# Optimization experiments

Hardware: AMD Instinct MI355X
Metric: run time of the kernel (lower is better)

The kernel has to match this reference:

```python
import jax, jax.numpy as jnp
import numpy as np

K = 3          # kernel size
PAD = 1        # padding


def _conv2d(x, w, b):
    # plain 3x3 conv, stride 1, pad 1, NCHW / OIHW
    out = jax.lax.conv_general_dilated(
        x, w, window_strides=(1, 1), padding=((PAD, PAD), (PAD, PAD)),
        dimension_numbers=('NCHW', 'OIHW', 'NCHW'))
    return out + b[None, :, None, None]


def _deform_conv2d(x, offsets, w, b):
    # torchvision deform_conv2d semantics (stride=1, dilation=1, no mask)
    B, C, H, W = x.shape
    K2 = K * K
    off = offsets.reshape(B, K2, 2, H, W)
    dy, dx = off[:, :, 0], off[:, :, 1]              # [B,K2,H,W], (y,x) order
    ki, kj = jnp.meshgrid(jnp.arange(K), jnp.arange(K), indexing='ij')
    ki = ki.reshape(K2).astype(x.dtype)
    kj = kj.reshape(K2).astype(x.dtype)
    base_y = (jnp.arange(H, dtype=x.dtype)[None, :, None] - PAD + ki[:, None, None])  # [K2,H,1]
    base_x = (jnp.arange(W, dtype=x.dtype)[None, None, :] - PAD + kj[:, None, None])  # [K2,1,W]
    py = base_y[None] + dy                            # [B,K2,H,W] sampling rows
    px = base_x[None] + dx                            # [B,K2,H,W] sampling cols

    y0 = jnp.floor(py); x0 = jnp.floor(px)
    y1 = y0 + 1.0;      x1 = x0 + 1.0
    wy1 = py - y0; wy0 = 1.0 - wy1
    wx1 = px - x0; wx0 = 1.0 - wx1

    def corner(yc, xc, wgt):
        valid = ((yc >= 0) & (yc <= H - 1) & (xc >= 0) & (xc <= W - 1))
        iy = jnp.clip(yc, 0, H - 1).astype(jnp.int32)
        ix = jnp.clip(xc, 0, W - 1).astype(jnp.int32)
        # per-batch gather: x[b][:, iy[b], ix[b]] -> [C,K2,H,W]
        vals = jax.vmap(lambda xb, iyb, ixb: xb[:, iyb, ixb])(x, iy, ix)
        return vals * (wgt * valid.astype(x.dtype))[:, None]  # [B,C,K2,H,W]

    sampled = (corner(y0, x0, wy0 * wx0) + corner(y0, x1, wy0 * wx1)
               + corner(y1, x0, wy1 * wx0) + corner(y1, x1, wy1 * wx1))
    out = jnp.einsum('bckhw,ock->bohw', sampled, w.reshape(w.shape[0], C, K2))
    return out + b[None, :, None, None]


def setup_inputs() -> dict:
    key = jax.random.key(0)
    ks = jax.random.split(key, 6)
    B, C, O, H, W = 4, 256, 256, 64, 64
    x = jax.random.normal(ks[0], (B, C, H, W), dtype=jnp.float32)
    y = jax.random.normal(ks[1], (B, C, H, W), dtype=jnp.float32)
    # offset conv predicts 2*K*K offset channels; small init keeps offsets a few px
    offset_w = jax.random.normal(ks[2], (2 * K * K, C, K, K), dtype=jnp.float32) * 0.01
    offset_b = jax.random.normal(ks[3], (2 * K * K,), dtype=jnp.float32) * 0.01
    deform_w = jax.random.normal(ks[4], (O, C, K, K), dtype=jnp.float32) * (1.0 / np.sqrt(C * K * K))
    deform_b = jax.random.normal(ks[5], (O,), dtype=jnp.float32) * 0.01
    return {"x": x, "y": y, "offset_w": offset_w, "offset_b": offset_b,
            "deform_w": deform_w, "deform_b": deform_b}


def reference(x, y, offset_w, offset_b, deform_w, deform_b):
    offsets = _conv2d(y, offset_w, offset_b)          # [B, 2*K*K, H, W]
    return _deform_conv2d(x, offsets, deform_w, deform_b)
```

## Files before the change

### kernel.cpp

```cpp
#include <hip/hip_runtime.h>
#include <hip/hip_bf16.h>
#include <stdint.h>


typedef __bf16 bf16x8 __attribute__((ext_vector_type(8)));
typedef float  f32x4  __attribute__((ext_vector_type(4)));

__device__ __forceinline__ unsigned short f2bfu(float f) {
    union { float f; unsigned u; } v; v.f = f;
    return (unsigned short)((v.u + 0x8000u) >> 16);
}
__device__ __forceinline__ float lo16(unsigned u) {
    union { unsigned u; float f; } v; v.u = u << 16; return v.f;
}
__device__ __forceinline__ float hi16(unsigned u) {
    union { unsigned u; float f; } v; v.u = u & 0xFFFF0000u; return v.f;
}
__device__ __forceinline__ unsigned fbits(float f) {
    union { float f; unsigned u; } v; v.f = f; return v.u;
}
__device__ __forceinline__ unsigned blend2(unsigned u0, unsigned u1, unsigned u2, unsigned u3,
                                           float4 w) {
    float lo = w.x * lo16(u0) + w.y * lo16(u1) + w.z * lo16(u2) + w.w * lo16(u3);
    float hi = w.x * hi16(u0) + w.y * hi16(u1) + w.z * hi16(u2) + w.w * hi16(u3);
    unsigned rl = fbits(lo) + 0x8000u;
    unsigned rh = fbits(hi) + 0x8000u;
    return __builtin_amdgcn_perm(rh, rl, 0x07060302);
}

__global__ __launch_bounds__(256) void xpose2_kernel(const float* __restrict__ x,
                                                     const float* __restrict__ y,
                                                     unsigned short* __restrict__ xT,
                                                     unsigned short* __restrict__ yT) {
    __shared__ float tile[64 * 69];
    int blk = blockIdx.x;
    const float* src = x; unsigned short* dst = xT;
    if (blk >= 1024) { src = y; dst = yT; blk -= 1024; }
    int cq = blk & 3;
    int bh = blk >> 2;
    int t = threadIdx.x;
    int w4 = t & 15, cl0 = t >> 4;
    const float* s = src + ((size_t)(bh >> 6) * 256 + cq * 64) * 4096 + (size_t)(bh & 63) * 64;
#pragma unroll
    for (int p = 0; p < 4; ++p) {
        int cl = p * 16 + cl0;
        float4 v = *(const float4*)&s[(size_t)cl * 4096 + w4 * 4];
        tile[(w4 * 4 + 0) * 69 + cl] = v.x;
        tile[(w4 * 4 + 1) * 69 + cl] = v.y;
        tile[(w4 * 4 + 2) * 69 + cl] = v.z;
        tile[(w4 * 4 + 3) * 69 + cl] = v.w;
    }
    __syncthreads();
    unsigned short* d = dst + (size_t)bh * 16384 + cq * 64;
#pragma unroll
    for (int p = 0; p < 4; ++p) {
        int w = p * 16 + cl0;
        float4 v = *(const float4*)&tile[w * 69 + w4 * 4];
        ushort4 r = make_ushort4(f2bfu(v.x), f2bfu(v.y), f2bfu(v.z), f2bfu(v.w));
        *(ushort4*)&d[w * 256 + w4 * 4] = r;
    }
}

__global__ __launch_bounds__(256) void packw_kernel(const float* __restrict__ dw,
                                                    unsigned short* __restrict__ Wp2) {
    int tid = blockIdx.x * 256 + threadIdx.x;
    int q8 = tid >> 8;
    int o  = tid & 255;
    int k0 = q8 * 8;
    int tap = k0 >> 8, c0 = k0 & 255;
    const float* s = dw + o * 2304 + c0 * 9 + tap;
    ushort4 r0 = make_ushort4(f2bfu(s[0]), f2bfu(s[9]), f2bfu(s[18]), f2bfu(s[27]));
    ushort4 r1 = make_ushort4(f2bfu(s[36]), f2bfu(s[45]), f2bfu(s[54]), f2bfu(s[63]));
    *(ushort4*)&Wp2[tid * 8 + 0] = r0;
    *(ushort4*)&Wp2[tid * 8 + 4] = r1;
}

__global__ __launch_bounds__(256) void packow_kernel(const float* __restrict__ ow,
                                                     unsigned short* __restrict__ Bo) {
    int idx = blockIdx.x * 256 + threadIdx.x;
    int j = idx & 7;
    int n = (idx >> 3) & 31;
    int lq = (idx >> 8) & 3;
    int kg = idx >> 10;
    int k = kg * 32 + lq * 8 + j;
    int tap = k >> 8, c = k & 255;
    float v = (n < 18) ? ow[n * 2304 + c * 9 + tap] : 0.f;
    Bo[idx] = f2bfu(v);
}

__global__ __launch_bounds__(512) void offs_mfma_kernel(
    const unsigned short* __restrict__ yT,
    const unsigned short* __restrict__ Bo,
    const float* __restrict__ ob,
    float* __restrict__ offs)
{
    __shared__ unsigned short yr[3 * 66 * 256];
    float* red = (float*)yr;

    int blk = blockIdx.x;
    int b = blk >> 6, h = blk & 63;
    int t = threadIdx.x;

#pragma unroll
    for (int r = 0; r < 3; ++r) {
        int hr = h + r - 1;
        bool rowok = (hr >= 0) && (hr < 64);
        const unsigned short* src = yT + (size_t)(b * 64 + (hr & 63)) * 64 * 256;
        for (int g = t; g < 2112; g += 512) {
            int wp = g >> 5, gi = g & 31;
            uint4 v = make_uint4(0, 0, 0, 0);
            if (rowok && wp >= 1 && wp <= 64)
                v = *(const uint4*)&src[(wp - 1) * 256 + gi * 8];
            *(uint4*)&yr[(r * 66 + wp) * 256 + (gi ^ (wp & 7)) * 8] = v;
        }
    }
    __syncthreads();

    int wv = t >> 6, lane = t & 63;
    int mh = wv & 1, kq = wv >> 1;
    int ln = lane & 15, lq = lane >> 4;

    f32x4 acc[2][2];
#pragma unroll
    for (int ms = 0; ms < 2; ++ms)
#pragma unroll
        for (int nt = 0; nt < 2; ++nt)
            acc[ms][nt] = (f32x4){0.f, 0.f, 0.f, 0.f};

    for (int u = kq; u < 72; u += 4) {
        int tap = u >> 3, kc = u & 7;
        int ki = tap / 3, kj = tap - ki * 3;
        int gb = kc * 4 + lq;
        bf16x8 af[2];
#pragma unroll
        for (int ms = 0; ms < 2; ++ms) {
            int wp = mh * 32 + ms * 16 + ln + kj;
            af[ms] = *(const bf16x8*)&yr[(ki * 66 + wp) * 256 + (gb ^ (wp & 7)) * 8];
        }
        bf16x8 bfr[2];
#pragma unroll
        for (int nt = 0; nt < 2; ++nt)
            bfr[nt] = *(const bf16x8*)&Bo[(tap * 8 + kc) * 1024 + lq * 256 + (nt * 16 + ln) * 8];
#pragma unroll
        for (int ms = 0; ms < 2; ++ms)
#pragma unroll
            for (int nt = 0; nt < 2; ++nt)
                acc[ms][nt] = __builtin_amdgcn_mfma_f32_16x16x32_bf16(af[ms], bfr[nt], acc[ms][nt], 0, 0, 0);
    }

    __syncthreads();
    if (kq > 0) {
        float* rg = red + (size_t)((mh * 3 + (kq - 1)) * 4) * 256;
#pragma unroll
        for (int ms = 0; ms < 2; ++ms)
#pragma unroll
            for (int nt = 0; nt < 2; ++nt)
#pragma unroll
                for (int r = 0; r < 4; ++r)
                    rg[(ms * 2 + nt) * 256 + (lq * 4 + r) * 16 + ln] = acc[ms][nt][r];
    }
    __syncthreads();
    if (kq == 0) {
#pragma unroll
        for (int ms = 0; ms < 2; ++ms)
#pragma unroll
            for (int nt = 0; nt < 2; ++nt) {
                int o = nt * 16 + ln;
                f32x4 s = acc[ms][nt];
#pragma unroll
                for (int kk = 0; kk < 3; ++kk) {
                    const float* rg = red + (size_t)((mh * 3 + kk) * 4 + ms * 2 + nt) * 256;
#pragma unroll
                    for (int r = 0; r < 4; ++r)
                        s[r] += rg[(lq * 4 + r) * 16 + ln];
                }
                if (o < 18) {
                    float bias = ob[o];
                    float* dst = offs + ((size_t)b * 18 + o) * 4096 + h * 64 + mh * 32 + ms * 16 + lq * 4;
                    float4 st = make_float4(s[0] + bias, s[1] + bias, s[2] + bias, s[3] + bias);
                    *(float4*)dst = st;
                }
            }
    }
}

__device__ __forceinline__ void gather_tap(const unsigned short* __restrict__ xtb,
                                           unsigned short* __restrict__ buf,
                                           const float4* __restrict__ pw_lds,
                                           const int4* __restrict__ pi_lds,
                                           int tap, int wv, int lane) {
    int p2 = lane >> 5, cl = lane & 31;
    int c0 = cl * 8;
    int base = tap * 64 + wv * 2 + p2;
    float4 w = pw_lds[base];
    int4  pi = pi_lds[base];
    uint4 a00 = *(const uint4*)&xtb[pi.x + c0];
    uint4 a01 = *(const uint4*)&xtb[pi.y + c0];
    uint4 a10 = *(const uint4*)&xtb[pi.z + c0];
    uint4 a11 = *(const uint4*)&xtb[pi.w + c0];
#pragma unroll
    for (int i = 0; i < 4; ++i) {
        uint4 b00, b01, b10, b11; float4 wn; int4 pin;
        if (i < 3) {
            wn  = pw_lds[base + (i + 1) * 16];
            pin = pi_lds[base + (i + 1) * 16];
            b00 = *(const uint4*)&xtb[pin.x + c0];
            b01 = *(const uint4*)&xtb[pin.y + c0];
            b10 = *(const uint4*)&xtb[pin.z + c0];
            b11 = *(const uint4*)&xtb[pin.w + c0];
        }
        int pos = i * 16 + wv * 2 + p2;
        uint4 res;
        res.x = blend2(a00.x, a01.x, a10.x, a11.x, w);
        res.y = blend2(a00.y, a01.y, a10.y, a11.y, w);
        res.z = blend2(a00.z, a01.z, a10.z, a11.z, w);
        res.w = blend2(a00.w, a01.w, a10.w, a11.w, w);
        *(uint4*)&buf[pos * 256 + (cl ^ (pos & 7)) * 8] = res;
        if (i < 3) { a00 = b00; a01 = b01; a10 = b10; a11 = b11; w = wn; pi = pin; }
    }
}

__global__ __launch_bounds__(512, 2) void deform_kernel(
    const unsigned short* __restrict__ xT,
    const unsigned short* __restrict__ Wp2,
    const float* __restrict__ offs,
    const float* __restrict__ db,
    float* __restrict__ out)
{
    __shared__ unsigned char smem[86016];
    unsigned short* Abuf0 = (unsigned short*)smem;
    unsigned short* Abuf1 = (unsigned short*)(smem + 32768);
    float* epi = (float*)smem;
    float4* pw_lds = (float4*)(smem + 67584);
    int4*   pi_lds = (int4*)(smem + 67584 + 9216);

    int blk = blockIdx.x;
    int b = blk >> 6, h = blk & 63;
    int t = threadIdx.x;
    int wv = t >> 6, lane = t & 63;
    int ln = lane & 15, lq = lane >> 4;
    int ns = wv & 3, kh = wv >> 2;

    const unsigned short* xtb = xT + (size_t)b * (64 * 64 * 256);
    const float* offb = offs + (size_t)b * 18 * 4096 + h * 64;

    for (int job = t; job < 576; job += 512) {
        int tap = job >> 6, pos = job & 63;
        int ki = tap / 3, kj = tap - ki * 3;
        float dy = offb[(tap * 2 + 0) * 4096 + pos];
        float dx = offb[(tap * 2 + 1) * 4096 + pos];
        float py = (float)(h - 1 + ki) + dy;
        float px = (float)(pos - 1 + kj) + dx;
        float y0 = floorf(py), x0 = floorf(px);
        float wy1 = py - y0, wx1 = px - x0;
        float wy0 = 1.f - wy1, wx0 = 1.f - wx1;
        float y1 = y0 + 1.f, x1 = x0 + 1.f;
        float vy0 = (y0 >= 0.f && y0 <= 63.f) ? 1.f : 0.f;
        float vy1 = (y1 >= 0.f && y1 <= 63.f) ? 1.f : 0.f;
        float vx0 = (x0 >= 0.f && x0 <= 63.f) ? 1.f : 0.f;
        float vx1 = (x1 >= 0.f && x1 <= 63.f) ? 1.f : 0.f;
        int iy0 = (int)fminf(fmaxf(y0, 0.f), 63.f);
        int iy1 = (int)fminf(fmaxf(y1, 0.f), 63.f);
        int ix0 = (int)fminf(fmaxf(x0, 0.f), 63.f);
        int ix1 = (int)fminf(fmaxf(x1, 0.f), 63.f);
        pw_lds[job] = make_float4(wy0 * wx0 * vy0 * vx0, wy0 * wx1 * vy0 * vx1,
                                  wy1 * wx0 * vy1 * vx0, wy1 * wx1 * vy1 * vx1);
        pi_lds[job] = make_int4((iy0 * 64 + ix0) * 256, (iy0 * 64 + ix1) * 256,
                                (iy1 * 64 + ix0) * 256, (iy1 * 64 + ix1) * 256);
    }
    __syncthreads();

    f32x4 acc[4][4];
#pragma unroll
    for (int ms = 0; ms < 4; ++ms)
#pragma unroll
        for (int nt = 0; nt < 4; ++nt)
            acc[ms][nt] = (f32x4){0.f, 0.f, 0.f, 0.f};

    gather_tap(xtb, Abuf0, pw_lds, pi_lds, 0, wv, lane);
    __syncthreads();

    for (int tap = 0; tap < 9; ++tap) {
        if (tap < 8)
            gather_tap(xtb, ((tap + 1) & 1) ? Abuf1 : Abuf0, pw_lds, pi_lds, tap + 1, wv, lane);
        const unsigned short* Ab = (tap & 1) ? Abuf1 : Abuf0;
#pragma unroll
        for (int kc = 0; kc < 4; ++kc) {
            int gbase = kh * 16 + kc * 4 + lq;
            bf16x8 af[4];
#pragma unroll
            for (int ms = 0; ms < 4; ++ms) {
                int row = ms * 16 + ln;
                af[ms] = *(const bf16x8*)&Ab[row * 256 + (gbase ^ (row & 7)) * 8];
            }
            int kg = tap * 8 + kh * 4 + kc;
            bf16x8 bfr[4];
#pragma unroll
            for (int nt = 0; nt < 4; ++nt)
                bfr[nt] = *(const bf16x8*)&Wp2[((kg * 4 + lq) * 256 + ns * 64 + nt * 16 + ln) * 8];
#pragma unroll
            for (int ms = 0; ms < 4; ++ms)
#pragma unroll
                for (int nt = 0; nt < 4; ++nt)
                    acc[ms][nt] = __builtin_amdgcn_mfma_f32_16x16x32_bf16(af[ms], bfr[nt], acc[ms][nt], 0, 0, 0);
        }
        __syncthreads();
    }

    if (kh == 1) {
        float* e = epi + (size_t)ns * 4224;
#pragma unroll
        for (int ms = 0; ms < 4; ++ms)
#pragma unroll
            for (int nt = 0; nt < 4; ++nt) {
                int o_l = nt * 16 + ln;
                int wb = ms * 16 + lq * 4;
                f32x4 a = acc[ms][nt];
                float4 st = make_float4(a[0], a[1], a[2], a[3]);
                *(float4*)&e[o_l * 66 + wb] = st;
            }
    }
    __syncthreads();
    if (kh == 0) {
        const float* e = epi + (size_t)ns * 4224;
#pragma unroll
        for (int ms = 0; ms < 4; ++ms)
#pragma unroll
            for (int nt = 0; nt < 4; ++nt) {
                int o_l = nt * 16 + ln;
                int o = ns * 64 + o_l;
                int wb = ms * 16 + lq * 4;
                float bias = db[o];
                float4 p = *(const float4*)&e[o_l * 66 + wb];
                f32x4 a = acc[ms][nt];
                float4 st = make_float4(a[0] + p.x + bias, a[1] + p.y + bias,
                                        a[2] + p.z + bias, a[3] + p.w + bias);
                *(float4*)&out[((size_t)(b * 256 + o)) * 4096 + h * 64 + wb] = st;
            }
    }
}

extern "C" void kernel_launch(void* const* d_in, const int* in_sizes, int n_in,
                              void* d_out, int out_size, void* d_ws, size_t ws_size,
                              hipStream_t stream) {
    const float* x  = (const float*)d_in[0];
    const float* y  = (const float*)d_in[1];
    const float* ow = (const float*)d_in[2];
    const float* ob = (const float*)d_in[3];
    const float* dw = (const float*)d_in[4];
    const float* db = (const float*)d_in[5];
    float* out = (float*)d_out;

    char* ws = (char*)d_ws;
    unsigned short* xT  = (unsigned short*)(ws);
    unsigned short* yT  = (unsigned short*)(ws + 8388608);
    unsigned short* Wp2 = (unsigned short*)(ws + 16777216);
    unsigned short* Bo  = (unsigned short*)(ws + 16777216 + 1179648);
    float*          offs = (float*)(ws + 16777216 + 1179648 + 147456);

    hipLaunchKernelGGL(xpose2_kernel, dim3(2048), dim3(256), 0, stream, x, y, xT, yT);
    hipLaunchKernelGGL(packw_kernel, dim3(288), dim3(256), 0, stream, dw, Wp2);
    hipLaunchKernelGGL(packow_kernel, dim3(288), dim3(256), 0, stream, ow, Bo);
    hipLaunchKernelGGL(offs_mfma_kernel, dim3(256), dim3(512), 0, stream, yT, Bo, ob, offs);
    hipLaunchKernelGGL(deform_kernel, dim3(256), dim3(512), 0, stream, xT, Wp2, offs, db, out);
}
```

Baseline: 144.3 us.

## Split rows into half-row blocks, merge prep kernels, restructure gather pipelining

Merges the transpose and weight-packing kernels into one prep launch. Both the offset conv and the deform conv now work on half-row tiles (32 positions), doubling the grid to 512 blocks with a swizzled block order, raising launch bounds to 4 blocks per CU and shrinking LDS use. The deform gather is split into an issue phase (global loads into registers before the MFMA loop) and a commit phase (blend and LDS write after it), so gather latency overlaps with compute. The epilogue uses an XOR-swizzled LDS layout. The trade-off is more tap-halo reloads per block and higher register pressure from holding the gathered values across the MFMA loop.

```diff
diff --git a/kernel.cpp b/kernel.cpp
--- a/kernel.cpp
+++ b/kernel.cpp
@@ -28,214 +28,190 @@
     return __builtin_amdgcn_perm(rh, rl, 0x07060302);
 }
 
-__global__ __launch_bounds__(256) void xpose2_kernel(const float* __restrict__ x,
-                                                     const float* __restrict__ y,
-                                                     unsigned short* __restrict__ xT,
-                                                     unsigned short* __restrict__ yT) {
+__global__ __launch_bounds__(256) void prep_kernel(
+    const float* __restrict__ x, const float* __restrict__ y,
+    const float* __restrict__ ow, const float* __restrict__ dw,
+    unsigned short* __restrict__ xT, unsigned short* __restrict__ yT,
+    unsigned short* __restrict__ Wp2, unsigned short* __restrict__ Bo)
+{
     __shared__ float tile[64 * 69];
     int blk = blockIdx.x;
-    const float* src = x; unsigned short* dst = xT;
-    if (blk >= 1024) { src = y; dst = yT; blk -= 1024; }
-    int cq = blk & 3;
-    int bh = blk >> 2;
     int t = threadIdx.x;
-    int w4 = t & 15, cl0 = t >> 4;
-    const float* s = src + ((size_t)(bh >> 6) * 256 + cq * 64) * 4096 + (size_t)(bh & 63) * 64;
-#pragma unroll
-    for (int p = 0; p < 4; ++p) {
-        int cl = p * 16 + cl0;
-        float4 v = *(const float4*)&s[(size_t)cl * 4096 + w4 * 4];
-        tile[(w4 * 4 + 0) * 69 + cl] = v.x;
-        tile[(w4 * 4 + 1) * 69 + cl] = v.y;
-        tile[(w4 * 4 + 2) * 69 + cl] = v.z;
-        tile[(w4 * 4 + 3) * 69 + cl] = v.w;
-    }
-    __syncthreads();
-    unsigned short* d = dst + (size_t)bh * 16384 + cq * 64;
-#pragma unroll
-    for (int p = 0; p < 4; ++p) {
-        int w = p * 16 + cl0;
-        float4 v = *(const float4*)&tile[w * 69 + w4 * 4];
-        ushort4 r = make_ushort4(f2bfu(v.x), f2bfu(v.y), f2bfu(v.z), f2bfu(v.w));
-        *(ushort4*)&d[w * 256 + w4 * 4] = r;
-    }
-}
-
-__global__ __launch_bounds__(256) void packw_kernel(const float* __restrict__ dw,
-                                                    unsigned short* __restrict__ Wp2) {
-    int tid = blockIdx.x * 256 + threadIdx.x;
-    int q8 = tid >> 8;
-    int o  = tid & 255;
-    int k0 = q8 * 8;
-    int tap = k0 >> 8, c0 = k0 & 255;
-    const float* s = dw + o * 2304 + c0 * 9 + tap;
-    ushort4 r0 = make_ushort4(f2bfu(s[0]), f2bfu(s[9]), f2bfu(s[18]), f2bfu(s[27]));
-    ushort4 r1 = make_ushort4(f2bfu(s[36]), f2bfu(s[45]), f2bfu(s[54]), f2bfu(s[63]));
-    *(ushort4*)&Wp2[tid * 8 + 0] = r0;
-    *(ushort4*)&Wp2[tid * 8 + 4] = r1;
-}
-
-__global__ __launch_bounds__(256) void packow_kernel(const float* __restrict__ ow,
-                                                     unsigned short* __restrict__ Bo) {
-    int idx = blockIdx.x * 256 + threadIdx.x;
-    int j = idx & 7;
-    int n = (idx >> 3) & 31;
-    int lq = (idx >> 8) & 3;
-    int kg = idx >> 10;
-    int k = kg * 32 + lq * 8 + j;
-    int tap = k >> 8, c = k & 255;
-    float v = (n < 18) ? ow[n * 2304 + c * 9 + tap] : 0.f;
-    Bo[idx] = f2bfu(v);
-}
-
-__global__ __launch_bounds__(512) void offs_mfma_kernel(
+    if (blk < 2048) {
+        const float* src = x; unsigned short* dst = xT;
+        if (blk >= 1024) { src = y; dst = yT; blk -= 1024; }
+        int cq = blk & 3;
+        int bh = blk >> 2;
+        int w4 = t & 15, cl0 = t >> 4;
+        const float* s = src + ((size_t)(bh >> 6) * 256 + cq * 64) * 4096 + (size_t)(bh & 63) * 64;
+#pragma unroll
+        for (int p = 0; p < 4; ++p) {
+            int cl = p * 16 + cl0;
+            float4 v = *(const float4*)&s[(size_t)cl * 4096 + w4 * 4];
+            tile[(w4 * 4 + 0) * 69 + cl] = v.x;
+            tile[(w4 * 4 + 1) * 69 + cl] = v.y;
+            tile[(w4 * 4 + 2) * 69 + cl] = v.z;
+            tile[(w4 * 4 + 3) * 69 + cl] = v.w;
+        }
+        __syncthreads();
+        unsigned short* d = dst + (size_t)bh * 16384 + cq * 64;
+#pragma unroll
+        for (int p = 0; p < 4; ++p) {
+            int w = p * 16 + cl0;
+            float4 v = *(const float4*)&tile[w * 69 + w4 * 4];
+            ushort4 r = make_ushort4(f2bfu(v.x), f2bfu(v.y), f2bfu(v.z), f2bfu(v.w));
+            *(ushort4*)&d[w * 256 + w4 * 4] = r;
+        }
+    } else if (blk < 2336) {
+        int tid = (blk - 2048) * 256 + t;
+        int q8 = tid >> 8;
+        int o  = tid & 255;
+        int k0 = q8 * 8;
+        int tap = k0 >> 8, c0 = k0 & 255;
+        const float* s = dw + o * 2304 + c0 * 9 + tap;
+        ushort4 r0 = make_ushort4(f2bfu(s[0]), f2bfu(s[9]), f2bfu(s[18]), f2bfu(s[27]));
+        ushort4 r1 = make_ushort4(f2bfu(s[36]), f2bfu(s[45]), f2bfu(s[54]), f2bfu(s[63]));
+        *(ushort4*)&Wp2[tid * 8 + 0] = r0;
+        *(ushort4*)&Wp2[tid * 8 + 4] = r1;
+    } else {
+        int idx = (blk - 2336) * 256 + t;
+        int j = idx & 7;
+        int n = (idx >> 3) & 31;
+        int lq = (idx >> 8) & 3;
+        int kg = idx >> 10;
+        int k = kg * 32 + lq * 8 + j;
+        int tap = k >> 8, c = k & 255;
+        float v = (n < 18) ? ow[n * 2304 + c * 9 + tap] : 0.f;
+        Bo[idx] = f2bfu(v);
+    }
+}
+
+__global__ __launch_bounds__(512, 4) void offs_mfma_kernel(
     const unsigned short* __restrict__ yT,
     const unsigned short* __restrict__ Bo,
     const float* __restrict__ ob,
     float* __restrict__ offs)
 {
-    __shared__ unsigned short yr[3 * 66 * 256];
-    float* red = (float*)yr;
+    __shared__ __align__(16) unsigned char ysm[52224];
+    unsigned short* yr = (unsigned short*)ysm;
+    float* red = (float*)ysm;
 
     int blk = blockIdx.x;
-    int b = blk >> 6, h = blk & 63;
+    int lb = (blk & 7) * 64 + (blk >> 3);
+    int b = lb >> 7, rem = lb & 127, h = rem >> 1, mh = rem & 1;
     int t = threadIdx.x;
 
-#pragma unroll
-    for (int r = 0; r < 3; ++r) {
-        int hr = h + r - 1;
-        bool rowok = (hr >= 0) && (hr < 64);
-        const unsigned short* src = yT + (size_t)(b * 64 + (hr & 63)) * 64 * 256;
-        for (int g = t; g < 2112; g += 512) {
-            int wp = g >> 5, gi = g & 31;
-            uint4 v = make_uint4(0, 0, 0, 0);
-            if (rowok && wp >= 1 && wp <= 64)
-                v = *(const uint4*)&src[(wp - 1) * 256 + gi * 8];
-            *(uint4*)&yr[(r * 66 + wp) * 256 + (gi ^ (wp & 7)) * 8] = v;
-        }
+    for (unsigned g = t; g < 3264; g += 512) {
+        unsigned r = g / 1088;
+        unsigned rm = g - r * 1088;
+        int wp = rm >> 5, gr = rm & 31;
+        int hr = h + (int)r - 1;
+        int w = mh * 32 + wp - 1;
+        uint4 v = make_uint4(0, 0, 0, 0);
+        if (hr >= 0 && hr < 64 && w >= 0 && w < 64)
+            v = *(const uint4*)&yT[((size_t)(b * 64 + hr) * 64 + w) * 256 + gr * 8];
+        *(uint4*)&yr[((r * 34) + wp) * 256 + (gr ^ (wp & 7)) * 8] = v;
     }
     __syncthreads();
 
     int wv = t >> 6, lane = t & 63;
-    int mh = wv & 1, kq = wv >> 1;
+    int kq = wv >> 1, m16 = wv & 1;
     int ln = lane & 15, lq = lane >> 4;
 
-    f32x4 acc[2][2];
-#pragma unroll
-    for (int ms = 0; ms < 2; ++ms)
-#pragma unroll
-        for (int nt = 0; nt < 2; ++nt)
-            acc[ms][nt] = (f32x4){0.f, 0.f, 0.f, 0.f};
+    f32x4 acc[2];
+    acc[0] = (f32x4){0.f, 0.f, 0.f, 0.f};
+    acc[1] = (f32x4){0.f, 0.f, 0.f, 0.f};
 
     for (int u = kq; u < 72; u += 4) {
         int tap = u >> 3, kc = u & 7;
         int ki = tap / 3, kj = tap - ki * 3;
-        int gb = kc * 4 + lq;
-        bf16x8 af[2];
-#pragma unroll
-        for (int ms = 0; ms < 2; ++ms) {
-            int wp = mh * 32 + ms * 16 + ln + kj;
-            af[ms] = *(const bf16x8*)&yr[(ki * 66 + wp) * 256 + (gb ^ (wp & 7)) * 8];
+        int wp = m16 * 16 + ln + kj;
+        bf16x8 af = *(const bf16x8*)&yr[(ki * 34 + wp) * 256 + ((kc * 4 + lq) ^ (wp & 7)) * 8];
+        bf16x8 b0 = *(const bf16x8*)&Bo[(tap * 8 + kc) * 1024 + lq * 256 + ln * 8];
+        bf16x8 b1 = *(const bf16x8*)&Bo[(tap * 8 + kc) * 1024 + lq * 256 + (16 + ln) * 8];
+        acc[0] = __builtin_amdgcn_mfma_f32_16x16x32_bf16(af, b0, acc[0], 0, 0, 0);
+        acc[1] = __builtin_amdgcn_mfma_f32_16x16x32_bf16(af, b1, acc[1], 0, 0, 0);
+    }
+
+    __syncthreads();
+    if (kq > 0) {
+        float* rg = red + (size_t)(((kq - 1) * 2 + m16) * 2) * 256;
+#pragma unroll
+        for (int nt = 0; nt < 2; ++nt)
+#pragma unroll
+            for (int r = 0; r < 4; ++r)
+                rg[nt * 256 + (lq * 4 + r) * 16 + ln] = acc[nt][r];
+    }
+    __syncthreads();
+    if (kq == 0) {
+#pragma unroll
+        for (int nt = 0; nt < 2; ++nt) {
+            int o = nt * 16 + ln;
+            f32x4 s = acc[nt];
+#pragma unroll
+            for (int kk = 0; kk < 3; ++kk) {
+                const float* rg = red + (size_t)((kk * 2 + m16) * 2 + nt) * 256;
+#pragma unroll
+                for (int r = 0; r < 4; ++r)
+                    s[r] += rg[(lq * 4 + r) * 16 + ln];
+            }
+            if (o < 18) {
+                float bias = ob[o];
+                float* dst = offs + ((size_t)b * 18 + o) * 4096 + h * 64 + mh * 32 + m16 * 16 + lq * 4;
+                *(float4*)dst = make_float4(s[0] + bias, s[1] + bias, s[2] + bias, s[3] + bias);
+            }
         }
-        bf16x8 bfr[2];
-#pragma unroll
-        for (int nt = 0; nt < 2; ++nt)
-            bfr[nt] = *(const bf16x8*)&Bo[(tap * 8 + kc) * 1024 + lq * 256 + (nt * 16 + ln) * 8];
-#pragma unroll
-        for (int ms = 0; ms < 2; ++ms)
-#pragma unroll
-            for (int nt = 0; nt < 2; ++nt)
-                acc[ms][nt] = __builtin_amdgcn_mfma_f32_16x16x32_bf16(af[ms], bfr[nt], acc[ms][nt], 0, 0, 0);
-    }
-
-    __syncthreads();
-    if (kq > 0) {
-        float* rg = red + (size_t)((mh * 3 + (kq - 1)) * 4) * 256;
-#pragma unroll
-        for (int ms = 0; ms < 2; ++ms)
-#pragma unroll
-            for (int nt = 0; nt < 2; ++nt)
-#pragma unroll
-                for (int r = 0; r < 4; ++r)
-                    rg[(ms * 2 + nt) * 256 + (lq * 4 + r) * 16 + ln] = acc[ms][nt][r];
-    }
-    __syncthreads();
-    if (kq == 0) {
-#pragma unroll
-        for (int ms = 0; ms < 2; ++ms)
-#pragma unroll
-            for (int nt = 0; nt < 2; ++nt) {
-                int o = nt * 16 + ln;
-                f32x4 s = acc[ms][nt];
-#pragma unroll
-                for (int kk = 0; kk < 3; ++kk) {
-                    const float* rg = red + (size_t)((mh * 3 + kk) * 4 + ms * 2 + nt) * 256;
-#pragma unroll
-                    for (int r = 0; r < 4; ++r)
-                        s[r] += rg[(lq * 4 + r) * 16 + ln];
-                }
-                if (o < 18) {
-                    float bias = ob[o];
-                    float* dst = offs + ((size_t)b * 18 + o) * 4096 + h * 64 + mh * 32 + ms * 16 + lq * 4;
-                    float4 st = make_float4(s[0] + bias, s[1] + bias, s[2] + bias, s[3] + bias);
-                    *(float4*)dst = st;
-                }
-            }
-    }
-}
-
-__device__ __forceinline__ void gather_tap(const unsigned short* __restrict__ xtb,
-                                           unsigned short* __restrict__ buf,
-                                           const float4* __restrict__ pw_lds,
-                                           const int4* __restrict__ pi_lds,
-                                           int tap, int wv, int lane) {
-    int p2 = lane >> 5, cl = lane & 31;
-    int c0 = cl * 8;
-    int base = tap * 64 + wv * 2 + p2;
-    float4 w = pw_lds[base];
-    int4  pi = pi_lds[base];
-    uint4 a00 = *(const uint4*)&xtb[pi.x + c0];
-    uint4 a01 = *(const uint4*)&xtb[pi.y + c0];
-    uint4 a10 = *(const uint4*)&xtb[pi.z + c0];
-    uint4 a11 = *(const uint4*)&xtb[pi.w + c0];
-#pragma unroll
-    for (int i = 0; i < 4; ++i) {
-        uint4 b00, b01, b10, b11; float4 wn; int4 pin;
-        if (i < 3) {
-            wn  = pw_lds[base + (i + 1) * 16];
-            pin = pi_lds[base + (i + 1) * 16];
-            b00 = *(const uint4*)&xtb[pin.x + c0];
-            b01 = *(const uint4*)&xtb[pin.y + c0];
-            b10 = *(const uint4*)&xtb[pin.z + c0];
-            b11 = *(const uint4*)&xtb[pin.w + c0];
-        }
-        int pos = i * 16 + wv * 2 + p2;
+    }
+}
+
+__device__ __forceinline__ void gather_issue(const unsigned short* __restrict__ xtb,
+                                             const float4* __restrict__ pw_lds,
+                                             const int4* __restrict__ pi_lds,
+                                             int tap, int t, uint4 a[2][4], float4 wr[2]) {
+    int gr = t & 31, c0 = gr * 8;
+#pragma unroll
+    for (int it = 0; it < 2; ++it) {
+        int pos = (t >> 5) + it * 16;
+        wr[it] = pw_lds[tap * 32 + pos];
+        int4 p = pi_lds[tap * 32 + pos];
+        a[it][0] = *(const uint4*)&xtb[p.x + c0];
+        a[it][1] = *(const uint4*)&xtb[p.y + c0];
+        a[it][2] = *(const uint4*)&xtb[p.z + c0];
+        a[it][3] = *(const uint4*)&xtb[p.w + c0];
+    }
+}
+__device__ __forceinline__ void gather_commit(unsigned short* __restrict__ buf,
+                                              int t, uint4 a[2][4], float4 wr[2]) {
+    int gr = t & 31;
+#pragma unroll
+    for (int it = 0; it < 2; ++it) {
+        int pos = (t >> 5) + it * 16;
         uint4 res;
-        res.x = blend2(a00.x, a01.x, a10.x, a11.x, w);
-        res.y = blend2(a00.y, a01.y, a10.y, a11.y, w);
-        res.z = blend2(a00.z, a01.z, a10.z, a11.z, w);
-        res.w = blend2(a00.w, a01.w, a10.w, a11.w, w);
-        *(uint4*)&buf[pos * 256 + (cl ^ (pos & 7)) * 8] = res;
-        if (i < 3) { a00 = b00; a01 = b01; a10 = b10; a11 = b11; w = wn; pi = pin; }
-    }
-}
-
-__global__ __launch_bounds__(512, 2) void deform_kernel(
+        res.x = blend2(a[it][0].x, a[it][1].x, a[it][2].x, a[it][3].x, wr[it]);
+        res.y = blend2(a[it][0].y, a[it][1].y, a[it][2].y, a[it][3].y, wr[it]);
+        res.z = blend2(a[it][0].z, a[it][1].z, a[it][2].z, a[it][3].z, wr[it]);
+        res.w = blend2(a[it][0].w, a[it][1].w, a[it][2].w, a[it][3].w, wr[it]);
+        *(uint4*)&buf[pos * 256 + (gr ^ (pos & 7)) * 8] = res;
+    }
+}
+
+__global__ __launch_bounds__(512, 4) void deform_kernel(
     const unsigned short* __restrict__ xT,
     const unsigned short* __restrict__ Wp2,
     const float* __restrict__ offs,
     const float* __restrict__ db,
     float* __restrict__ out)
 {
-    __shared__ unsigned char smem[86016];
+    __shared__ __align__(16) unsigned char smem[41984];
     unsigned short* Abuf0 = (unsigned short*)smem;
-    unsigned short* Abuf1 = (unsigned short*)(smem + 32768);
-    float* epi = (float*)smem;
-    float4* pw_lds = (float4*)(smem + 67584);
-    int4*   pi_lds = (int4*)(smem + 67584 + 9216);
+    unsigned short* Abuf1 = (unsigned short*)(smem + 16384);
+    float4* pw_lds = (float4*)(smem + 32768);
+    int4*   pi_lds = (int4*)(smem + 32768 + 4608);
+    float*  epi    = (float*)smem;
 
     int blk = blockIdx.x;
-    int b = blk >> 6, h = blk & 63;
+    int lb = (blk & 7) * 64 + (blk >> 3);
+    int b = lb >> 7, rem = lb & 127, h = rem >> 1, mh = rem & 1;
     int t = threadIdx.x;
     int wv = t >> 6, lane = t & 63;
     int ln = lane & 15, lq = lane >> 4;
@@ -244,13 +220,14 @@
     const unsigned short* xtb = xT + (size_t)b * (64 * 64 * 256);
     const float* offb = offs + (size_t)b * 18 * 4096 + h * 64;
 
-    for (int job = t; job < 576; job += 512) {
-        int tap = job >> 6, pos = job & 63;
+    if (t < 288) {
+        int tap = t >> 5, pos_l = t & 31;
+        int pos_g = mh * 32 + pos_l;
         int ki = tap / 3, kj = tap - ki * 3;
-        float dy = offb[(tap * 2 + 0) * 4096 + pos];
-        float dx = offb[(tap * 2 + 1) * 4096 + pos];
+        float dy = offb[(tap * 2 + 0) * 4096 + pos_g];
+        float dx = offb[(tap * 2 + 1) * 4096 + pos_g];
         float py = (float)(h - 1 + ki) + dy;
-        float px = (float)(pos - 1 + kj) + dx;
+        float px = (float)(pos_g - 1 + kj) + dx;
         float y0 = floorf(py), x0 = floorf(px);
         float wy1 = py - y0, wx1 = px - x0;
         float wy0 = 1.f - wy1, wx0 = 1.f - wx1;
@@ -263,35 +240,36 @@
         int iy1 = (int)fminf(fmaxf(y1, 0.f), 63.f);
         int ix0 = (int)fminf(fmaxf(x0, 0.f), 63.f);
         int ix1 = (int)fminf(fmaxf(x1, 0.f), 63.f);
-        pw_lds[job] = make_float4(wy0 * wx0 * vy0 * vx0, wy0 * wx1 * vy0 * vx1,
-                                  wy1 * wx0 * vy1 * vx0, wy1 * wx1 * vy1 * vx1);
-        pi_lds[job] = make_int4((iy0 * 64 + ix0) * 256, (iy0 * 64 + ix1) * 256,
-                                (iy1 * 64 + ix0) * 256, (iy1 * 64 + ix1) * 256);
-    }
-    __syncthreads();
-
-    f32x4 acc[4][4];
-#pragma unroll
-    for (int ms = 0; ms < 4; ++ms)
+        pw_lds[t] = make_float4(wy0 * wx0 * vy0 * vx0, wy0 * wx1 * vy0 * vx1,
+                                wy1 * wx0 * vy1 * vx0, wy1 * wx1 * vy1 * vx1);
+        pi_lds[t] = make_int4((iy0 * 64 + ix0) * 256, (iy0 * 64 + ix1) * 256,
+                              (iy1 * 64 + ix0) * 256, (iy1 * 64 + ix1) * 256);
+    }
+    __syncthreads();
+
+    f32x4 acc[2][4];
+#pragma unroll
+    for (int ms = 0; ms < 2; ++ms)
 #pragma unroll
         for (int nt = 0; nt < 4; ++nt)
             acc[ms][nt] = (f32x4){0.f, 0.f, 0.f, 0.f};
 
-    gather_tap(xtb, Abuf0, pw_lds, pi_lds, 0, wv, lane);
+    uint4 ga[2][4]; float4 gw[2];
+    gather_issue(xtb, pw_lds, pi_lds, 0, t, ga, gw);
+    gather_commit(Abuf0, t, ga, gw);
     __syncthreads();
 
     for (int tap = 0; tap < 9; ++tap) {
         if (tap < 8)
-            gather_tap(xtb, ((tap + 1) & 1) ? Abuf1 : Abuf0, pw_lds, pi_lds, tap + 1, wv, lane);
+            gather_issue(xtb, pw_lds, pi_lds, tap + 1, t, ga, gw);
         const unsigned short* Ab = (tap & 1) ? Abuf1 : Abuf0;
 #pragma unroll
         for (int kc = 0; kc < 4; ++kc) {
-            int gbase = kh * 16 + kc * 4 + lq;
-            bf16x8 af[4];
-#pragma unroll
-            for (int ms = 0; ms < 4; ++ms) {
+            bf16x8 af[2];
+#pragma unroll
+            for (int ms = 0; ms < 2; ++ms) {
                 int row = ms * 16 + ln;
-                af[ms] = *(const bf16x8*)&Ab[row * 256 + (gbase ^ (row & 7)) * 8];
+                af[ms] = *(const bf16x8*)&Ab[row * 256 + (((kh * 16 + kc * 4 + lq)) ^ (row & 7)) * 8];
             }
             int kg = tap * 8 + kh * 4 + kc;
             bf16x8 bfr[4];
@@ -299,40 +277,42 @@
             for (int nt = 0; nt < 4; ++nt)
                 bfr[nt] = *(const bf16x8*)&Wp2[((kg * 4 + lq) * 256 + ns * 64 + nt * 16 + ln) * 8];
 #pragma unroll
-            for (int ms = 0; ms < 4; ++ms)
+            for (int ms = 0; ms < 2; ++ms)
 #pragma unroll
                 for (int nt = 0; nt < 4; ++nt)
                     acc[ms][nt] = __builtin_amdgcn_mfma_f32_16x16x32_bf16(af[ms], bfr[nt], acc[ms][nt], 0, 0, 0);
         }
+        if (tap < 8)
+            gather_commit((tap & 1) ? Abuf0 : Abuf1, t, ga, gw);
         __syncthreads();
     }
 
     if (kh == 1) {
-        float* e = epi + (size_t)ns * 4224;
-#pragma unroll
-        for (int ms = 0; ms < 4; ++ms)
+        float* e = epi + (size_t)ns * 2048;
+#pragma unroll
+        for (int ms = 0; ms < 2; ++ms)
 #pragma unroll
             for (int nt = 0; nt < 4; ++nt) {
                 int o_l = nt * 16 + ln;
-                int wb = ms * 16 + lq * 4;
+                int g = (ms * 4 + lq) ^ (o_l & 7);
                 f32x4 a = acc[ms][nt];
-                float4 st = make_float4(a[0], a[1], a[2], a[3]);
-                *(float4*)&e[o_l * 66 + wb] = st;
+                *(float4*)&e[o_l * 32 + g * 4] = make_float4(a[0], a[1], a[2], a[3]);
             }
     }
     __syncthreads();
     if (kh == 0) {
-        const float* e = epi + (size_t)ns * 4224;
-#pragma unroll
-        for (int ms = 0; ms < 4; ++ms)
+        const float* e = epi + (size_t)ns * 2048;
+#pragma unroll
+        for (int ms = 0; ms < 2; ++ms)
 #pragma unroll
             for (int nt = 0; nt < 4; ++nt) {
                 int o_l = nt * 16 + ln;
                 int o = ns * 64 + o_l;
-                int wb = ms * 16 + lq * 4;
+                int g = (ms * 4 + lq) ^ (o_l & 7);
                 float bias = db[o];
-                float4 p = *(const float4*)&e[o_l * 66 + wb];
+                float4 p = *(const float4*)&e[o_l * 32 + g * 4];
                 f32x4 a = acc[ms][nt];
+                int wb = mh * 32 + ms * 16 + lq * 4;
                 float4 st = make_float4(a[0] + p.x + bias, a[1] + p.y + bias,
                                         a[2] + p.z + bias, a[3] + p.w + bias);
                 *(float4*)&out[((size_t)(b * 256 + o)) * 4096 + h * 64 + wb] = st;
@@ -358,9 +338,8 @@
     unsigned short* Bo  = (unsigned short*)(ws + 16777216 + 1179648);
     float*          offs = (float*)(ws + 16777216 + 1179648 + 147456);
 
-    hipLaunchKernelGGL(xpose2_kernel, dim3(2048), dim3(256), 0, stream, x, y, xT, yT);
-    hipLaunchKernelGGL(packw_kernel, dim3(288), dim3(256), 0, stream, dw, Wp2);
-    hipLaunchKernelGGL(packow_kernel, dim3(288), dim3(256), 0, stream, ow, Bo);
-    hipLaunchKernelGGL(offs_mfma_kernel, dim3(256), dim3(512), 0, stream, yT, Bo, ob, offs);
-    hipLaunchKernelGGL(deform_kernel, dim3(256), dim3(512), 0, stream, xT, Wp2, offs, db, out);
-}
+    hipLaunchKernelGGL(prep_kernel, dim3(2624), dim3(256), 0, stream,
+                       x, y, ow, dw, xT, yT, Wp2, Bo);
+    hipLaunchKernelGGL(offs_mfma_kernel, dim3(512), dim3(512), 0, stream, yT, Bo, ob, offs);
+    hipLaunchKernelGGL(deform_kernel, dim3(512), dim3(512), 0, stream, xT, Wp2, offs, db, out);
+}
```

Result: faster. 137.4 us (-4.8%).
